# Optimization experiments

Hardware: AMD Instinct MI355X
Metric: run time of the kernel (lower is better)

Reference implementation:

```python
import jax, jax.numpy as jnp
import numpy as np

B, C, H, W = 32, 128, 56, 56
KSEL = 2            # gate columns (experts selected per sample)
E = 8               # expert_per_task
KN = 128            # kernel_num
KS = 3              # kernel_size
PAD = (KS - 1) // 2


def setup_inputs() -> dict:
    key = jax.random.key(0)
    k1, k2, k3, k4 = jax.random.split(key, 4)
    x = jax.random.normal(k1, (B, C, H, W), dtype=jnp.float32)
    gate = jax.random.randint(k2, (B, KSEL), 0, E, dtype=jnp.int32)
    conv_special_param = jax.random.normal(k3, (E, KN, C, KS, KS), dtype=jnp.float32) * 0.05
    conv_channel_param = jax.random.normal(k4, (E, C, C + KN, 1, 1), dtype=jnp.float32) * 0.05
    return {"x": x, "gate": gate,
            "conv_special_param": conv_special_param,
            "conv_channel_param": conv_channel_param}


def _per_sample_conv(xb, wb):
    # xb: [C, H+2p, W+2p], wb: [KN, C, KS, KS] -> [KN, H, W]
    out = jax.lax.conv_general_dilated(
        xb[None], wb, window_strides=(1, 1), padding='VALID',
        dimension_numbers=('NCHW', 'OIHW', 'NCHW'))
    return out[0]


def reference(x, gate, conv_special_param, conv_channel_param):
    px = jnp.pad(x, ((0, 0), (0, 0), (PAD, PAD), (PAD, PAD)))

    def per_gate(idx):  # idx: [B] expert indices for this gate column
        w_spec = conv_special_param[idx]                 # [B, KN, C, KS, KS]
        nf = jax.vmap(_per_sample_conv)(px, w_spec)      # [B, KN, H, W]
        cated = jnp.concatenate([x, nf], axis=1)         # [B, C+KN, H, W]
        w_ch = conv_channel_param[idx][..., 0, 0]        # [B, C, C+KN]
        return jnp.einsum('boc,bchw->bohw', w_ch, cated)  # [B, C, H, W]

    # stack over gate columns -> [B, KSEL, C, H, W]
    return jax.vmap(per_gate, in_axes=1, out_axes=1)(gate)
```

## Files before the change

kernel.cpp:

```cpp
#include <hip/hip_runtime.h>
#include <hip/hip_bf16.h>

#define B_   32
#define C_   128
#define H_   56
#define W_   56
#define KSEL 2
#define E_   8
#define KN_  128

typedef __attribute__((ext_vector_type(8))) short short8;
typedef __attribute__((ext_vector_type(4))) float f32x4;

static __device__ __forceinline__ ushort f2bf(float f) {
  union { float f; uint u; } v; v.f = f;
  uint u = v.u;
  return (ushort)((u + 0x7fffu + ((u >> 16) & 1u)) >> 16);
}

#define CELL_US 40
#define ROW_US  2560
#define ROW_B   5120
#define REG_B   30720

__global__ __launch_bounds__(256) void prep_x_kernel(
    const float* __restrict__ x, ushort* __restrict__ xh) {
  const int hp = blockIdx.x;
  const int b  = blockIdx.y;
  const int tid = threadIdx.x;

  if (hp == 0 || hp == 57) {
    uint4 z = make_uint4(0, 0, 0, 0);
#pragma unroll
    for (int cc = 0; cc < 4; ++cc) {
      ushort* rp = xh + ((size_t)(b * 4 + cc) * 58 + hp) * ROW_US;
      for (int l = tid; l < 320; l += 256) ((uint4*)rp)[l] = z;
    }
    return;
  }
  const int h = hp - 1;
  __shared__ __align__(16) ushort sT[56 * 136];

  const float* xb = x + (size_t)b * C_ * H_ * W_ + h * W_;
#pragma unroll
  for (int it = 0; it < 7; ++it) {
    int i4 = tid + it * 256;
    int c  = i4 / 14;
    int w4 = (i4 - c * 14) * 4;
    float4 v = *(const float4*)(xb + (size_t)c * (H_ * W_) + w4);
    sT[(w4 + 0) * 136 + c] = f2bf(v.x);
    sT[(w4 + 1) * 136 + c] = f2bf(v.y);
    sT[(w4 + 2) * 136 + c] = f2bf(v.z);
    sT[(w4 + 3) * 136 + c] = f2bf(v.w);
  }
  __syncthreads();
  for (int q = tid; q < 1280; q += 256) {
    int cc  = q / 320, rem = q - cc * 320;
    int cell = rem / 5, sub = rem - cell * 5;
    uint4 v = make_uint4(0, 0, 0, 0);
    if (sub < 4 && cell >= 1 && cell <= 56)
      v = *(const uint4*)&sT[(cell - 1) * 136 + cc * 32 + sub * 8];
    ushort* rp = xh + ((size_t)(b * 4 + cc) * 58 + hp) * ROW_US;
    *(uint4*)(rp + cell * CELL_US + sub * 8) = v;
  }
}

__global__ __launch_bounds__(256) void fuse_weights_kernel(
    const float* __restrict__ Ws,
    const float* __restrict__ Wch,
    ushort* __restrict__ Weff) {
  const int e  = blockIdx.x;
  const int o0 = blockIdx.y * 32;
  const int c0 = blockIdx.z * 32;
  const int tid = threadIdx.x;
  const int ol = tid >> 3;
  const int cq = (tid & 7) * 4;

  __shared__ __align__(16) float sA[32 * 129];
  __shared__ __align__(16) float sB[32 * 32 * 12];

#pragma unroll
  for (int it = 0; it < 4; ++it) {
    int i4 = tid + it * 256;
    int o  = i4 >> 5;
    int kk = (i4 & 31) * 4;
    float4 v = *(const float4*)(Wch + (size_t)(e * C_ + o0 + o) * 256 + 128 + kk);
    sA[o * 129 + kk + 0] = v.x;
    sA[o * 129 + kk + 1] = v.y;
    sA[o * 129 + kk + 2] = v.z;
    sA[o * 129 + kk + 3] = v.w;
  }

  float acc[9][4];
#pragma unroll
  for (int j = 0; j < 9; ++j)
#pragma unroll
    for (int c2 = 0; c2 < 4; ++c2) acc[j][c2] = 0.f;

  for (int k0 = 0; k0 < 128; k0 += 32) {
    __syncthreads();
    {
      int k = tid >> 3, seg = tid & 7;
      const float* src = Ws + ((size_t)(e * KN_ + k0 + k) * C_ + c0) * 9 + seg * 36;
      float vb[36];
#pragma unroll
      for (int q = 0; q < 9; ++q) {
        float4 v = *(const float4*)(src + q * 4);
        vb[q * 4 + 0] = v.x; vb[q * 4 + 1] = v.y;
        vb[q * 4 + 2] = v.z; vb[q * 4 + 3] = v.w;
      }
      int c = seg * 4, j = 0;
#pragma unroll
      for (int m = 0; m < 36; ++m) {
        sB[(k * 32 + c) * 12 + j] = vb[m];
        if (++j == 9) { j = 0; ++c; }
      }
    }
    __syncthreads();
    for (int k = 0; k < 32; ++k) {
      float a = sA[ol * 129 + k0 + k];
#pragma unroll
      for (int c2 = 0; c2 < 4; ++c2) {
        const float* bp = &sB[(k * 32 + cq + c2) * 12];
#pragma unroll
        for (int j = 0; j < 9; ++j) acc[j][c2] += a * bp[j];
      }
    }
  }

  const int o = o0 + ol;
#pragma unroll
  for (int c2 = 0; c2 < 4; ++c2)
    acc[4][c2] += Wch[(size_t)(e * C_ + o) * 256 + c0 + cq + c2];

  const int nt   = (o0 >> 4) + (ol >> 4);
  const int lane = ((cq >> 3) << 4) | (ol & 15);
#pragma unroll
  for (int j = 0; j < 9; ++j) {
    uint lo = (uint)f2bf(acc[j][0]) | ((uint)f2bf(acc[j][1]) << 16);
    uint hi = (uint)f2bf(acc[j][2]) | ((uint)f2bf(acc[j][3]) << 16);
    size_t base = ((((size_t)(e * 9 + j) * 8 + nt) * 4 + blockIdx.z) * 64 + lane) * 8
                  + (cq & 4);
    *(uint2*)(Weff + base) = make_uint2(lo, hi);
  }
}

#define OSTR 228

#define BAR() do { asm volatile("" ::: "memory"); \
                   __builtin_amdgcn_s_barrier();  \
                   asm volatile("" ::: "memory"); } while (0)

__global__ __launch_bounds__(256, 2) void conv_mfma_kernel(
    const ushort* __restrict__ xh,
    const int* __restrict__ gate,
    const ushort* __restrict__ Weff,
    float* __restrict__ out) {
  const int P   = blockIdx.x;
  const int xcd = P & 7;
  const int s   = P >> 3;
  const int bl  = s / 28;
  const int r1  = s - bl * 28;
  const int g   = r1 / 14;
  const int ht  = r1 - g * 14;
  const int b   = xcd * 4 + bl;
  const int bg  = b * 2 + g;
  const int h0  = ht * 4;
  const int e   = gate[bg];

  const int tid = threadIdx.x;
  const int wv = tid >> 6, lane = tid & 63;
  const int l15 = lane & 15, kq = lane >> 4;
  const int mh = wv >> 1, nh = wv & 1;

  __shared__ __align__(128) char smem[2 * REG_B];
  ushort* bufA = (ushort*)smem;
  ushort* bufB = (ushort*)(smem + REG_B);

  f32x4 acc[7][4];
#pragma unroll
  for (int t = 0; t < 7; ++t)
#pragma unroll
    for (int i = 0; i < 4; ++i) acc[t][i] = (f32x4){0.f, 0.f, 0.f, 0.f};

  int addr0[7];
#pragma unroll
  for (int t = 0; t < 7; ++t) {
    int p = mh * 112 + t * 16 + l15;
    int r = p / 56;
    int w = p - r * 56;
    addr0[t] = (r * 64 + w) * CELL_US + kq * 8;
  }

  const char* xbase = (const char*)xh;
#define STAGE(cc, dst) do {                                                   \
    const char* srp = xbase + ((size_t)((b * 4 + (cc)) * 58 + h0)) * ROW_B    \
                            + lane * 16;                                      \
    char* drp = (char*)(dst);                                                 \
    _Pragma("unroll")                                                         \
    for (int it_ = 0; it_ < 8; ++it_) {                                       \
      int n_ = wv + it_ * 4;                                                  \
      if (n_ < 30)                                                            \
        __builtin_amdgcn_global_load_lds(                                     \
            (const __attribute__((address_space(1))) unsigned int*)(srp + n_ * 1024), \
            (__attribute__((address_space(3))) unsigned int*)(drp + n_ * 1024),       \
            16, 0, 0);                                                        \
    }                                                                         \
  } while (0)

  const ushort* wlane = Weff + (size_t)e * (9 * 8 * 4 * 64 * 8)
                             + (size_t)(nh * 4) * (4 * 64 * 8)
                             + (size_t)lane * 8;

#define COMPUTE(sXb, cc) do {                                                 \
    _Pragma("unroll")                                                         \
    for (int dy = 0; dy < 3; ++dy) {                                          \
      _Pragma("unroll")                                                       \
      for (int dx = 0; dx < 3; ++dx) {                                        \
        const int j_ = dy * 3 + dx;                                           \
        short8 bfr[4];                                                        \
        _Pragma("unroll")                                                     \
        for (int i = 0; i < 4; ++i)                                           \
          bfr[i] = *(const short8*)(wlane + (size_t)j_ * (8 * 4 * 64 * 8)     \
                                          + (size_t)i * (4 * 64 * 8)          \
                                          + (size_t)(cc) * (64 * 8));         \
        const int ao = (dy * 64 + dx) * CELL_US;                              \
        _Pragma("unroll")                                                     \
        for (int t = 0; t < 7; ++t) {                                         \
          short8 a = *(const short8*)&(sXb)[addr0[t] + ao];                   \
          _Pragma("unroll")                                                   \
          for (int i = 0; i < 4; ++i)                                         \
            acc[t][i] = __builtin_amdgcn_mfma_f32_16x16x32_bf16(              \
                a, bfr[i], acc[t][i], 0, 0, 0);                               \
        }                                                                     \
      }                                                                       \
    }                                                                         \
  } while (0)

  STAGE(0, bufA);
  STAGE(1, bufB);
  asm volatile("s_waitcnt vmcnt(30)" ::: "memory");
  BAR();
  COMPUTE(bufA, 0);
  BAR();
  STAGE(2, bufA);
  asm volatile("s_waitcnt vmcnt(30)" ::: "memory");
  BAR();
  COMPUTE(bufB, 1);
  BAR();
  STAGE(3, bufB);
  asm volatile("s_waitcnt vmcnt(30)" ::: "memory");
  BAR();
  COMPUTE(bufA, 2);
  BAR();
  asm volatile("s_waitcnt vmcnt(0)" ::: "memory");
  BAR();
  COMPUTE(bufB, 3);

  float* sO = (float*)bufA;
  for (int gq = 0; gq < 4; ++gq) {
    if (nh == (gq >> 1)) {
      const int gg = gq & 1;
#pragma unroll
      for (int ii = 0; ii < 2; ++ii) {
        const int i = gg * 2 + ii;
#pragma unroll
        for (int t = 0; t < 7; ++t) {
          int p0 = mh * 112 + t * 16 + kq * 4;
          int r  = p0 / 56;
          int w0 = p0 - r * 56;
          *(float4*)&sO[(ii * 16 + l15) * OSTR + r * 56 + w0] =
              make_float4(acc[t][i][0], acc[t][i][1], acc[t][i][2], acc[t][i][3]);
        }
      }
    }
    __syncthreads();
    {
      float* ob = out + ((size_t)bg * C_ + 32 * gq) * (H_ * W_) + (size_t)h0 * W_;
#pragma unroll
      for (int k = 0; k < 7; ++k) {
        int idx = k * 256 + tid;
        int ol  = idx / 56;
        int pos = idx - ol * 56;
        float4 v = *(const float4*)&sO[ol * OSTR + pos * 4];
        *(float4*)(ob + (size_t)ol * (H_ * W_) + pos * 4) = v;
      }
    }
    __syncthreads();
  }
}

extern "C" void kernel_launch(void* const* d_in, const int* in_sizes, int n_in,
                              void* d_out, int out_size, void* d_ws, size_t ws_size,
                              hipStream_t stream) {
  const float* x    = (const float*)d_in[0];
  const int*   gate = (const int*)d_in[1];
  const float* Ws   = (const float*)d_in[2];
  const float* Wch  = (const float*)d_in[3];
  float* out = (float*)d_out;

  ushort* xh   = (ushort*)d_ws;
  ushort* Weff = xh + (size_t)32 * 4 * 58 * ROW_US;

  dim3 g0(58, 32);
  prep_x_kernel<<<g0, 256, 0, stream>>>(x, xh);

  dim3 g1(8, 4, 4);
  fuse_weights_kernel<<<g1, 256, 0, stream>>>(Ws, Wch, Weff);

  dim3 g2(896);
  conv_mfma_kernel<<<g2, 256, 0, stream>>>(xh, gate, Weff, out);
}
```

Before: 234.8 us.

## Compact padded activation layout with XOR-style swizzle and merge prep kernels

Shrinks each padded activation cell from 40 to 32 bf16 and uses a rotated quad order based on the cell index instead of padding to avoid LDS bank conflicts. This reduces the staged LDS buffers from 30 KB to 24 KB so three blocks per CU fit (launch bounds raised to 3), and cuts the async loads per stage. The two preprocessing kernels are merged into one launch, and weight fusion is retiled into smaller, more numerous blocks. The extra occupancy raises register pressure, since the 28 accumulator vectors now have to fit in a tighter per-wave budget.

```diff
diff --git a/kernel.cpp b/kernel.cpp
--- a/kernel.cpp
+++ b/kernel.cpp
@@ -18,130 +18,105 @@
   return (ushort)((u + 0x7fffu + ((u >> 16) & 1u)) >> 16);
 }
 
-#define CELL_US 40
-#define ROW_US  2560
-#define ROW_B   5120
-#define REG_B   30720
-
-__global__ __launch_bounds__(256) void prep_x_kernel(
-    const float* __restrict__ x, ushort* __restrict__ xh) {
-  const int hp = blockIdx.x;
-  const int b  = blockIdx.y;
-  const int tid = threadIdx.x;
-
-  if (hp == 0 || hp == 57) {
-    uint4 z = make_uint4(0, 0, 0, 0);
-#pragma unroll
-    for (int cc = 0; cc < 4; ++cc) {
-      ushort* rp = xh + ((size_t)(b * 4 + cc) * 58 + hp) * ROW_US;
-      for (int l = tid; l < 320; l += 256) ((uint4*)rp)[l] = z;
-    }
-    return;
-  }
-  const int h = hp - 1;
-  __shared__ __align__(16) ushort sT[56 * 136];
-
-  const float* xb = x + (size_t)b * C_ * H_ * W_ + h * W_;
-#pragma unroll
-  for (int it = 0; it < 7; ++it) {
-    int i4 = tid + it * 256;
-    int c  = i4 / 14;
-    int w4 = (i4 - c * 14) * 4;
-    float4 v = *(const float4*)(xb + (size_t)c * (H_ * W_) + w4);
-    sT[(w4 + 0) * 136 + c] = f2bf(v.x);
-    sT[(w4 + 1) * 136 + c] = f2bf(v.y);
-    sT[(w4 + 2) * 136 + c] = f2bf(v.z);
-    sT[(w4 + 3) * 136 + c] = f2bf(v.w);
-  }
-  __syncthreads();
-  for (int q = tid; q < 1280; q += 256) {
-    int cc  = q / 320, rem = q - cc * 320;
-    int cell = rem / 5, sub = rem - cell * 5;
-    uint4 v = make_uint4(0, 0, 0, 0);
-    if (sub < 4 && cell >= 1 && cell <= 56)
-      v = *(const uint4*)&sT[(cell - 1) * 136 + cc * 32 + sub * 8];
-    ushort* rp = xh + ((size_t)(b * 4 + cc) * 58 + hp) * ROW_US;
-    *(uint4*)(rp + cell * CELL_US + sub * 8) = v;
-  }
-}
-
-__global__ __launch_bounds__(256) void fuse_weights_kernel(
+#define CELL_US 32
+#define ROW_US  1856
+#define PLANE_US (58 * ROW_US)
+#define STAGE_B 24576
+
+__global__ __launch_bounds__(256) void prep_fuse_kernel(
+    const float* __restrict__ x,
     const float* __restrict__ Ws,
     const float* __restrict__ Wch,
+    ushort* __restrict__ xh,
     ushort* __restrict__ Weff) {
-  const int e  = blockIdx.x;
-  const int o0 = blockIdx.y * 32;
-  const int c0 = blockIdx.z * 32;
+  __shared__ __align__(16) char smem[27008];
+  const int q = blockIdx.x;
   const int tid = threadIdx.x;
-  const int ol = tid >> 3;
-  const int cq = (tid & 7) * 4;
-
-  __shared__ __align__(16) float sA[32 * 129];
-  __shared__ __align__(16) float sB[32 * 32 * 12];
-
-#pragma unroll
-  for (int it = 0; it < 4; ++it) {
-    int i4 = tid + it * 256;
-    int o  = i4 >> 5;
-    int kk = (i4 & 31) * 4;
-    float4 v = *(const float4*)(Wch + (size_t)(e * C_ + o0 + o) * 256 + 128 + kk);
-    sA[o * 129 + kk + 0] = v.x;
-    sA[o * 129 + kk + 1] = v.y;
-    sA[o * 129 + kk + 2] = v.z;
-    sA[o * 129 + kk + 3] = v.w;
-  }
-
-  float acc[9][4];
-#pragma unroll
-  for (int j = 0; j < 9; ++j)
-#pragma unroll
-    for (int c2 = 0; c2 < 4; ++c2) acc[j][c2] = 0.f;
-
-  for (int k0 = 0; k0 < 128; k0 += 32) {
+
+  if (q < 1856) {
+    const int b = q / 58, hp = q - (q / 58) * 58;
+    if (hp == 0 || hp == 57) {
+      uint4 z = make_uint4(0, 0, 0, 0);
+#pragma unroll
+      for (int cc = 0; cc < 4; ++cc) {
+        ushort* rp = xh + (size_t)(b * 4 + cc) * PLANE_US + (size_t)hp * ROW_US;
+        for (int l = tid; l < 232; l += 256) ((uint4*)rp)[l] = z;
+      }
+      return;
+    }
+    const int h = hp - 1;
+    ushort* sT = (ushort*)smem;
+    const float* xb = x + (size_t)b * C_ * H_ * W_ + h * W_;
+#pragma unroll
+    for (int it = 0; it < 7; ++it) {
+      int i4 = tid + it * 256;
+      int c  = i4 / 14;
+      int w4 = (i4 - c * 14) * 4;
+      float4 v = *(const float4*)(xb + (size_t)c * (H_ * W_) + w4);
+      sT[(w4 + 0) * 136 + c] = f2bf(v.x);
+      sT[(w4 + 1) * 136 + c] = f2bf(v.y);
+      sT[(w4 + 2) * 136 + c] = f2bf(v.z);
+      sT[(w4 + 3) * 136 + c] = f2bf(v.w);
+    }
     __syncthreads();
-    {
-      int k = tid >> 3, seg = tid & 7;
-      const float* src = Ws + ((size_t)(e * KN_ + k0 + k) * C_ + c0) * 9 + seg * 36;
-      float vb[36];
-#pragma unroll
-      for (int q = 0; q < 9; ++q) {
-        float4 v = *(const float4*)(src + q * 4);
-        vb[q * 4 + 0] = v.x; vb[q * 4 + 1] = v.y;
-        vb[q * 4 + 2] = v.z; vb[q * 4 + 3] = v.w;
-      }
-      int c = seg * 4, j = 0;
-#pragma unroll
-      for (int m = 0; m < 36; ++m) {
-        sB[(k * 32 + c) * 12 + j] = vb[m];
-        if (++j == 9) { j = 0; ++c; }
-      }
-    }
-    __syncthreads();
-    for (int k = 0; k < 32; ++k) {
-      float a = sA[ol * 129 + k0 + k];
-#pragma unroll
-      for (int c2 = 0; c2 < 4; ++c2) {
-        const float* bp = &sB[(k * 32 + cq + c2) * 12];
-#pragma unroll
-        for (int j = 0; j < 9; ++j) acc[j][c2] += a * bp[j];
-      }
-    }
-  }
-
-  const int o = o0 + ol;
-#pragma unroll
-  for (int c2 = 0; c2 < 4; ++c2)
-    acc[4][c2] += Wch[(size_t)(e * C_ + o) * 256 + c0 + cq + c2];
-
-  const int nt   = (o0 >> 4) + (ol >> 4);
-  const int lane = ((cq >> 3) << 4) | (ol & 15);
-#pragma unroll
-  for (int j = 0; j < 9; ++j) {
-    uint lo = (uint)f2bf(acc[j][0]) | ((uint)f2bf(acc[j][1]) << 16);
-    uint hi = (uint)f2bf(acc[j][2]) | ((uint)f2bf(acc[j][3]) << 16);
-    size_t base = ((((size_t)(e * 9 + j) * 8 + nt) * 4 + blockIdx.z) * 64 + lane) * 8
-                  + (cq & 4);
-    *(uint2*)(Weff + base) = make_uint2(lo, hi);
+    for (int m = tid; m < 928; m += 256) {
+      int cc   = m / 232, rem = m - cc * 232;
+      int cell = rem >> 2, qd = rem & 3;
+      uint4 v = make_uint4(0, 0, 0, 0);
+      if (cell >= 1 && cell <= 56)
+        v = *(const uint4*)&sT[(cell - 1) * 136 + cc * 32 + qd * 8];
+      int pq = (qd + (cell >> 1)) & 3;
+      ushort* rp = xh + (size_t)(b * 4 + cc) * PLANE_US + (size_t)hp * ROW_US;
+      *(uint4*)(rp + cell * CELL_US + pq * 8) = v;
+    }
+  } else {
+    const int fid = q - 1856;
+    const int e  = fid >> 6;
+    const int o0 = ((fid >> 3) & 7) << 4;
+    const int c0 = (fid & 7) << 4;
+    float* sA = (float*)smem;
+    float* sB = (float*)(smem + 16 * 132 * 4);
+
+    for (int m = tid; m < 512; m += 256) {
+      int o = m >> 5, kk = (m & 31) * 4;
+      float4 v = *(const float4*)(Wch + (size_t)(e * C_ + o0 + o) * 256 + 128 + kk);
+      sA[o * 132 + kk + 0] = v.x;
+      sA[o * 132 + kk + 1] = v.y;
+      sA[o * 132 + kk + 2] = v.z;
+      sA[o * 132 + kk + 3] = v.w;
+    }
+
+    const int orr = tid >> 4, cl = tid & 15;
+    float acc[9];
+#pragma unroll
+    for (int j = 0; j < 9; ++j) acc[j] = 0.f;
+
+    for (int k0 = 0; k0 < 128; k0 += 32) {
+      __syncthreads();
+      for (int m = tid; m < 1152; m += 256) {
+        int k = m / 36, f4 = m - k * 36;
+        float4 v = *(const float4*)(Ws + ((size_t)(e * KN_ + k0 + k) * C_ + c0) * 9 + f4 * 4);
+        *(float4*)&sB[k * 144 + f4 * 4] = v;
+      }
+      __syncthreads();
+      for (int k = 0; k < 32; ++k) {
+        float a = sA[orr * 132 + k0 + k];
+        const float* bp = &sB[k * 144 + cl * 9];
+#pragma unroll
+        for (int j = 0; j < 9; ++j) acc[j] += a * bp[j];
+      }
+    }
+
+    const int o = o0 + orr, c = c0 + cl;
+    acc[4] += Wch[(size_t)(e * C_ + o) * 256 + c];
+    const int nt   = o >> 4;
+    const int ct   = c >> 5;
+    const int lane = (((c >> 3) & 3) << 4) | (o & 15);
+#pragma unroll
+    for (int j = 0; j < 9; ++j) {
+      size_t base = ((((size_t)(e * 9 + j) * 8 + nt) * 4 + ct) * 64 + lane) * 8 + (c & 7);
+      Weff[base] = f2bf(acc[j]);
+    }
   }
 }
 
@@ -151,7 +126,7 @@
                    __builtin_amdgcn_s_barrier();  \
                    asm volatile("" ::: "memory"); } while (0)
 
-__global__ __launch_bounds__(256, 2) void conv_mfma_kernel(
+__global__ __launch_bounds__(256, 3) void conv_mfma_kernel(
     const ushort* __restrict__ xh,
     const int* __restrict__ gate,
     const ushort* __restrict__ Weff,
@@ -173,9 +148,9 @@
   const int l15 = lane & 15, kq = lane >> 4;
   const int mh = wv >> 1, nh = wv & 1;
 
-  __shared__ __align__(128) char smem[2 * REG_B];
+  __shared__ __align__(128) char smem[2 * STAGE_B];
   ushort* bufA = (ushort*)smem;
-  ushort* bufB = (ushort*)(smem + REG_B);
+  ushort* bufB = (ushort*)(smem + STAGE_B);
 
   f32x4 acc[7][4];
 #pragma unroll
@@ -183,28 +158,31 @@
 #pragma unroll
     for (int i = 0; i < 4; ++i) acc[t][i] = (f32x4){0.f, 0.f, 0.f, 0.f};
 
-  int addr0[7];
+  int axy[7][3];
 #pragma unroll
   for (int t = 0; t < 7; ++t) {
     int p = mh * 112 + t * 16 + l15;
     int r = p / 56;
     int w = p - r * 56;
-    addr0[t] = (r * 64 + w) * CELL_US + kq * 8;
+#pragma unroll
+    for (int dx = 0; dx < 3; ++dx) {
+      int cell = w + dx;
+      axy[t][dx] = r * ROW_US + cell * CELL_US + (((kq + (cell >> 1)) & 3) * 8);
+    }
   }
 
   const char* xbase = (const char*)xh;
 #define STAGE(cc, dst) do {                                                   \
-    const char* srp = xbase + ((size_t)((b * 4 + (cc)) * 58 + h0)) * ROW_B    \
-                            + lane * 16;                                      \
+    const char* srp = xbase + ((size_t)(b * 4 + (cc)) * PLANE_US              \
+                             + (size_t)h0 * ROW_US) * 2 + lane * 16;          \
     char* drp = (char*)(dst);                                                 \
     _Pragma("unroll")                                                         \
-    for (int it_ = 0; it_ < 8; ++it_) {                                       \
-      int n_ = wv + it_ * 4;                                                  \
-      if (n_ < 30)                                                            \
-        __builtin_amdgcn_global_load_lds(                                     \
-            (const __attribute__((address_space(1))) unsigned int*)(srp + n_ * 1024), \
-            (__attribute__((address_space(3))) unsigned int*)(drp + n_ * 1024),       \
-            16, 0, 0);                                                        \
+    for (int it_ = 0; it_ < 6; ++it_) {                                       \
+      int n_ = wv + it_ * 4;                    \
+      __builtin_amdgcn_global_load_lds(                                       \
+          (const __attribute__((address_space(1))) unsigned int*)(srp + n_ * 1024), \
+          (__attribute__((address_space(3))) unsigned int*)(drp + n_ * 1024),       \
+          16, 0, 0);                                                          \
     }                                                                         \
   } while (0)
 
@@ -224,10 +202,9 @@
           bfr[i] = *(const short8*)(wlane + (size_t)j_ * (8 * 4 * 64 * 8)     \
                                           + (size_t)i * (4 * 64 * 8)          \
                                           + (size_t)(cc) * (64 * 8));         \
-        const int ao = (dy * 64 + dx) * CELL_US;                              \
         _Pragma("unroll")                                                     \
         for (int t = 0; t < 7; ++t) {                                         \
-          short8 a = *(const short8*)&(sXb)[addr0[t] + ao];                   \
+          short8 a = *(const short8*)&(sXb)[axy[t][dx] + dy * ROW_US];        \
           _Pragma("unroll")                                                   \
           for (int i = 0; i < 4; ++i)                                         \
             acc[t][i] = __builtin_amdgcn_mfma_f32_16x16x32_bf16(              \
@@ -239,25 +216,25 @@
 
   STAGE(0, bufA);
   STAGE(1, bufB);
-  asm volatile("s_waitcnt vmcnt(30)" ::: "memory");
+  asm volatile("s_waitcnt vmcnt(6)" ::: "memory");
   BAR();
   COMPUTE(bufA, 0);
   BAR();
   STAGE(2, bufA);
-  asm volatile("s_waitcnt vmcnt(30)" ::: "memory");
+  asm volatile("s_waitcnt vmcnt(6)" ::: "memory");
   BAR();
   COMPUTE(bufB, 1);
   BAR();
   STAGE(3, bufB);
-  asm volatile("s_waitcnt vmcnt(30)" ::: "memory");
+  asm volatile("s_waitcnt vmcnt(6)" ::: "memory");
   BAR();
   COMPUTE(bufA, 2);
-  BAR();
   asm volatile("s_waitcnt vmcnt(0)" ::: "memory");
   BAR();
   COMPUTE(bufB, 3);
-
-  float* sO = (float*)bufA;
+  BAR();
+
+  float* sO = (float*)smem;
   for (int gq = 0; gq < 4; ++gq) {
     if (nh == (gq >> 1)) {
       const int gg = gq & 1;
@@ -300,13 +277,10 @@
   float* out = (float*)d_out;
 
   ushort* xh   = (ushort*)d_ws;
-  ushort* Weff = xh + (size_t)32 * 4 * 58 * ROW_US;
-
-  dim3 g0(58, 32);
-  prep_x_kernel<<<g0, 256, 0, stream>>>(x, xh);
-
-  dim3 g1(8, 4, 4);
-  fuse_weights_kernel<<<g1, 256, 0, stream>>>(Ws, Wch, Weff);
+  ushort* Weff = xh + (size_t)(32 * 4) * PLANE_US;
+
+  dim3 g0(1856 + 512);
+  prep_fuse_kernel<<<g0, 256, 0, stream>>>(x, Ws, Wch, xh, Weff);
 
   dim3 g2(896);
   conv_mfma_kernel<<<g2, 256, 0, stream>>>(xh, gate, Weff, out);
```

Result: slower. 427.2 us (+81.9%).

## Merge input prep and weight fusion into one launch with finer weight tiles

Applied to the files above, without the earlier changes.

Combines the x-to-bf16 transpose/pad kernel and the weight-fusion kernel into a single launch, with block index ranges selecting the role. The weight-fusion part now uses 16-channel tiles (256 blocks instead of 128) and coalesced float4 staging of Ws into shared memory. This removes one kernel launch and lets the small weight GEMM overlap with the x preparation. The cost is a larger shared allocation per block, which can lower occupancy for the prep blocks.

```diff
diff --git a/kernel.cpp b/kernel.cpp
--- a/kernel.cpp
+++ b/kernel.cpp
@@ -23,125 +23,109 @@
 #define ROW_B   5120
 #define REG_B   30720
 
-__global__ __launch_bounds__(256) void prep_x_kernel(
-    const float* __restrict__ x, ushort* __restrict__ xh) {
-  const int hp = blockIdx.x;
-  const int b  = blockIdx.y;
-  const int tid = threadIdx.x;
-
-  if (hp == 0 || hp == 57) {
-    uint4 z = make_uint4(0, 0, 0, 0);
-#pragma unroll
-    for (int cc = 0; cc < 4; ++cc) {
-      ushort* rp = xh + ((size_t)(b * 4 + cc) * 58 + hp) * ROW_US;
-      for (int l = tid; l < 320; l += 256) ((uint4*)rp)[l] = z;
-    }
-    return;
-  }
-  const int h = hp - 1;
-  __shared__ __align__(16) ushort sT[56 * 136];
-
-  const float* xb = x + (size_t)b * C_ * H_ * W_ + h * W_;
-#pragma unroll
-  for (int it = 0; it < 7; ++it) {
-    int i4 = tid + it * 256;
-    int c  = i4 / 14;
-    int w4 = (i4 - c * 14) * 4;
-    float4 v = *(const float4*)(xb + (size_t)c * (H_ * W_) + w4);
-    sT[(w4 + 0) * 136 + c] = f2bf(v.x);
-    sT[(w4 + 1) * 136 + c] = f2bf(v.y);
-    sT[(w4 + 2) * 136 + c] = f2bf(v.z);
-    sT[(w4 + 3) * 136 + c] = f2bf(v.w);
-  }
-  __syncthreads();
-  for (int q = tid; q < 1280; q += 256) {
-    int cc  = q / 320, rem = q - cc * 320;
-    int cell = rem / 5, sub = rem - cell * 5;
-    uint4 v = make_uint4(0, 0, 0, 0);
-    if (sub < 4 && cell >= 1 && cell <= 56)
-      v = *(const uint4*)&sT[(cell - 1) * 136 + cc * 32 + sub * 8];
-    ushort* rp = xh + ((size_t)(b * 4 + cc) * 58 + hp) * ROW_US;
-    *(uint4*)(rp + cell * CELL_US + sub * 8) = v;
-  }
-}
-
-__global__ __launch_bounds__(256) void fuse_weights_kernel(
+__global__ __launch_bounds__(256) void prep_fuse_kernel(
+    const float* __restrict__ x,
     const float* __restrict__ Ws,
     const float* __restrict__ Wch,
+    ushort* __restrict__ xh,
     ushort* __restrict__ Weff) {
-  const int e  = blockIdx.x;
-  const int o0 = blockIdx.y * 32;
-  const int c0 = blockIdx.z * 32;
+  __shared__ __align__(16) char smem[35456];
+  const int q = blockIdx.x;
   const int tid = threadIdx.x;
-  const int ol = tid >> 3;
-  const int cq = (tid & 7) * 4;
-
-  __shared__ __align__(16) float sA[32 * 129];
-  __shared__ __align__(16) float sB[32 * 32 * 12];
-
-#pragma unroll
-  for (int it = 0; it < 4; ++it) {
-    int i4 = tid + it * 256;
-    int o  = i4 >> 5;
-    int kk = (i4 & 31) * 4;
-    float4 v = *(const float4*)(Wch + (size_t)(e * C_ + o0 + o) * 256 + 128 + kk);
-    sA[o * 129 + kk + 0] = v.x;
-    sA[o * 129 + kk + 1] = v.y;
-    sA[o * 129 + kk + 2] = v.z;
-    sA[o * 129 + kk + 3] = v.w;
-  }
-
-  float acc[9][4];
-#pragma unroll
-  for (int j = 0; j < 9; ++j)
-#pragma unroll
-    for (int c2 = 0; c2 < 4; ++c2) acc[j][c2] = 0.f;
-
-  for (int k0 = 0; k0 < 128; k0 += 32) {
+
+  if (q < 1856) {
+    const int b = q / 58, hp = q - (q / 58) * 58;
+    if (hp == 0 || hp == 57) {
+      uint4 z = make_uint4(0, 0, 0, 0);
+#pragma unroll
+      for (int cc = 0; cc < 4; ++cc) {
+        ushort* rp = xh + ((size_t)(b * 4 + cc) * 58 + hp) * ROW_US;
+        for (int l = tid; l < 320; l += 256) ((uint4*)rp)[l] = z;
+      }
+      return;
+    }
+    const int h = hp - 1;
+    ushort* sT = (ushort*)smem;
+    const float* xb = x + (size_t)b * C_ * H_ * W_ + h * W_;
+#pragma unroll
+    for (int it = 0; it < 7; ++it) {
+      int i4 = tid + it * 256;
+      int c  = i4 / 14;
+      int w4 = (i4 - c * 14) * 4;
+      float4 v = *(const float4*)(xb + (size_t)c * (H_ * W_) + w4);
+      sT[(w4 + 0) * 136 + c] = f2bf(v.x);
+      sT[(w4 + 1) * 136 + c] = f2bf(v.y);
+      sT[(w4 + 2) * 136 + c] = f2bf(v.z);
+      sT[(w4 + 3) * 136 + c] = f2bf(v.w);
+    }
     __syncthreads();
-    {
-      int k = tid >> 3, seg = tid & 7;
-      const float* src = Ws + ((size_t)(e * KN_ + k0 + k) * C_ + c0) * 9 + seg * 36;
-      float vb[36];
-#pragma unroll
-      for (int q = 0; q < 9; ++q) {
-        float4 v = *(const float4*)(src + q * 4);
-        vb[q * 4 + 0] = v.x; vb[q * 4 + 1] = v.y;
-        vb[q * 4 + 2] = v.z; vb[q * 4 + 3] = v.w;
-      }
-      int c = seg * 4, j = 0;
-#pragma unroll
-      for (int m = 0; m < 36; ++m) {
-        sB[(k * 32 + c) * 12 + j] = vb[m];
-        if (++j == 9) { j = 0; ++c; }
-      }
-    }
-    __syncthreads();
-    for (int k = 0; k < 32; ++k) {
-      float a = sA[ol * 129 + k0 + k];
-#pragma unroll
-      for (int c2 = 0; c2 < 4; ++c2) {
-        const float* bp = &sB[(k * 32 + cq + c2) * 12];
-#pragma unroll
-        for (int j = 0; j < 9; ++j) acc[j][c2] += a * bp[j];
-      }
-    }
-  }
-
-  const int o = o0 + ol;
-#pragma unroll
-  for (int c2 = 0; c2 < 4; ++c2)
-    acc[4][c2] += Wch[(size_t)(e * C_ + o) * 256 + c0 + cq + c2];
-
-  const int nt   = (o0 >> 4) + (ol >> 4);
-  const int lane = ((cq >> 3) << 4) | (ol & 15);
-#pragma unroll
-  for (int j = 0; j < 9; ++j) {
-    uint lo = (uint)f2bf(acc[j][0]) | ((uint)f2bf(acc[j][1]) << 16);
-    uint hi = (uint)f2bf(acc[j][2]) | ((uint)f2bf(acc[j][3]) << 16);
-    size_t base = ((((size_t)(e * 9 + j) * 8 + nt) * 4 + blockIdx.z) * 64 + lane) * 8
-                  + (cq & 4);
-    *(uint2*)(Weff + base) = make_uint2(lo, hi);
+    for (int m = tid; m < 1280; m += 256) {
+      int cc   = m / 320, rem = m - cc * 320;
+      int cell = rem / 5, sub = rem - cell * 5;
+      uint4 v = make_uint4(0, 0, 0, 0);
+      if (sub < 4 && cell >= 1 && cell <= 56)
+        v = *(const uint4*)&sT[(cell - 1) * 136 + cc * 32 + sub * 8];
+      ushort* rp = xh + ((size_t)(b * 4 + cc) * 58 + hp) * ROW_US;
+      *(uint4*)(rp + cell * CELL_US + sub * 8) = v;
+    }
+  } else {
+    const int fid = q - 1856;
+    const int e  = fid >> 5;
+    const int o0 = ((fid >> 3) & 3) * 32;
+    const int c0 = (fid & 7) * 16;
+    float* sA = (float*)smem;
+    float* sB = (float*)(smem + 32 * 129 * 4);
+
+    for (int m = tid; m < 1024; m += 256) {
+      int o = m >> 5, kk = (m & 31) * 4;
+      float4 v = *(const float4*)(Wch + (size_t)(e * C_ + o0 + o) * 256 + 128 + kk);
+      sA[o * 129 + kk + 0] = v.x;
+      sA[o * 129 + kk + 1] = v.y;
+      sA[o * 129 + kk + 2] = v.z;
+      sA[o * 129 + kk + 3] = v.w;
+    }
+
+    const int o  = tid >> 3;
+    const int cp = (tid & 7) * 2;
+    float acc[9][2];
+#pragma unroll
+    for (int j = 0; j < 9; ++j) { acc[j][0] = 0.f; acc[j][1] = 0.f; }
+
+    for (int k0 = 0; k0 < 128; k0 += 32) {
+      __syncthreads();
+      for (int m = tid; m < 1152; m += 256) {
+        int k = m / 36, f4 = m - k * 36;
+        float4 v = *(const float4*)(Ws + ((size_t)(e * KN_ + k0 + k) * C_ + c0) * 9 + f4 * 4);
+        *(float4*)&sB[k * 148 + f4 * 4] = v;
+      }
+      __syncthreads();
+      for (int k = 0; k < 32; ++k) {
+        float a = sA[o * 129 + k0 + k];
+#pragma unroll
+        for (int c2 = 0; c2 < 2; ++c2) {
+          const float* bp = &sB[k * 148 + (cp + c2) * 9];
+#pragma unroll
+          for (int j = 0; j < 9; ++j) acc[j][c2] += a * bp[j];
+        }
+      }
+    }
+
+    const int og  = o0 + o;
+    const int cg0 = c0 + cp;
+#pragma unroll
+    for (int c2 = 0; c2 < 2; ++c2)
+      acc[4][c2] += Wch[(size_t)(e * C_ + og) * 256 + cg0 + c2];
+
+    const int nt   = og >> 4;
+    const int ct5  = cg0 >> 5;
+    const int lane = (((cg0 >> 3) & 3) << 4) | (og & 15);
+#pragma unroll
+    for (int j = 0; j < 9; ++j) {
+      uint w = (uint)f2bf(acc[j][0]) | ((uint)f2bf(acc[j][1]) << 16);
+      size_t base = ((((size_t)(e * 9 + j) * 8 + nt) * 4 + ct5) * 64 + lane) * 8
+                    + (cg0 & 7);
+      *(uint*)(Weff + base) = w;
+    }
   }
 }
 
@@ -302,11 +286,8 @@
   ushort* xh   = (ushort*)d_ws;
   ushort* Weff = xh + (size_t)32 * 4 * 58 * ROW_US;
 
-  dim3 g0(58, 32);
-  prep_x_kernel<<<g0, 256, 0, stream>>>(x, xh);
-
-  dim3 g1(8, 4, 4);
-  fuse_weights_kernel<<<g1, 256, 0, stream>>>(Ws, Wch, Weff);
+  dim3 g0(1856 + 256);
+  prep_fuse_kernel<<<g0, 256, 0, stream>>>(x, Ws, Wch, xh, Weff);
 
   dim3 g2(896);
   conv_mfma_kernel<<<g2, 256, 0, stream>>>(xh, gate, Weff, out);
```

Result: no change. 232.3 us (-1.1%).
